# Optimization experiments

Hardware: AMD Instinct MI355X
Metric: run time of the kernel (lower is better)

## Reference

```python
import jax, jax.numpy as jnp
import numpy as np

EMBED_DIM = 1024
NUM_HEADS = 16
D_K = EMBED_DIM // NUM_HEADS
BATCH, SEQ = 4, 2048


def setup_inputs() -> dict:
    key = jax.random.key(0)
    ks = jax.random.split(key, 6)
    s = 1.0 / np.sqrt(EMBED_DIM)
    return {
        "x": jax.random.normal(ks[0], (BATCH, SEQ, EMBED_DIM), dtype=jnp.float32),
        "mask": jnp.ones((BATCH, SEQ), dtype=jnp.int32),
        "Wq": jax.random.uniform(ks[1], (EMBED_DIM, EMBED_DIM), jnp.float32, -s, s),
        "Wk": jax.random.uniform(ks[2], (EMBED_DIM, EMBED_DIM), jnp.float32, -s, s),
        "Wv": jax.random.uniform(ks[3], (EMBED_DIM, EMBED_DIM), jnp.float32, -s, s),
        "Wo": jax.random.uniform(ks[4], (EMBED_DIM, EMBED_DIM), jnp.float32, -s, s),
    }


def reference(x, mask, Wq, Wk, Wv, Wo):
    B, S, E = x.shape
    H, Dk = NUM_HEADS, D_K
    # nn.Linear: y = x @ W.T ; reshape to [B, H, S, Dk]
    def proj(W):
        return jnp.einsum('bse,fe->bsf', x, W).reshape(B, S, H, Dk).transpose(0, 2, 1, 3)
    q, k, v = proj(Wq), proj(Wk), proj(Wv)
    scores = jnp.einsum('bhqd,bhkd->bhqk', q, k) / jnp.sqrt(jnp.float32(Dk))
    # key-padding mask: [B, S] -> [B, 1, 1, S]; 0 means masked with -inf
    scores = jnp.where(mask[:, None, None, :] == 0, -jnp.inf, scores)
    attn = jax.nn.softmax(scores, axis=-1)  # dropout is identity (p=0 / eval)
    out = jnp.einsum('bhqk,bhkd->bhqd', attn, v)
    out = out.transpose(0, 2, 1, 3).reshape(B, S, E)
    return jnp.einsum('bse,fe->bsf', out, Wo)
```

## Files before the change

### kernel.cpp

```cpp
#include <hip/hip_runtime.h>

typedef __attribute__((ext_vector_type(8))) __bf16   bf16x8;
typedef __attribute__((ext_vector_type(8))) _Float16 f16x8;
typedef __attribute__((ext_vector_type(4))) float    f32x4;

#define MFMA_BF16 __builtin_amdgcn_mfma_f32_16x16x32_bf16
#define MFMA_F16  __builtin_amdgcn_mfma_f32_16x16x32_f16

__global__ __launch_bounds__(256)
void cast_bf16(const float* __restrict__ src, __bf16* __restrict__ dst, int n8)
{
    int i = blockIdx.x * 256 + threadIdx.x;
    if (i >= n8) return;
    float4 v0 = *(const float4*)(src + (size_t)i * 8);
    float4 v1 = *(const float4*)(src + (size_t)i * 8 + 4);
    float xs[8] = {v0.x, v0.y, v0.z, v0.w, v1.x, v1.y, v1.z, v1.w};
    bf16x8 h8;
    #pragma unroll
    for (int j = 0; j < 8; j++) h8[j] = (__bf16)xs[j];
    *(bf16x8*)(dst + (size_t)i * 8) = h8;
}

#define GEMM_DECLS                                                          \
    __shared__ __bf16 Ah[128][40], Bh[128][40];                             \
    const int t    = threadIdx.x;                                           \
    const int lane = t & 63;                                                \
    const int wid  = t >> 6;                                                \
    const int l15  = lane & 15;                                             \
    const int lg   = lane >> 4;                                             \
    const int wr   = wid >> 1, wc = wid & 1;

#define GEMM_LOOP(Ag, Bg, m0, brow0, K)                                     \
    f32x4 acc[4][4];                                                        \
    _Pragma("unroll")                                                       \
    for (int i = 0; i < 4; i++)                                             \
        _Pragma("unroll")                                                   \
        for (int jj = 0; jj < 4; jj++)                                      \
            _Pragma("unroll")                                               \
            for (int r = 0; r < 4; r++) acc[i][jj][r] = 0.f;                \
    for (int k0 = 0; k0 < K; k0 += 32) {                                    \
        __syncthreads();                                                    \
        _Pragma("unroll")                                                   \
        for (int i = 0; i < 2; i++) {                                       \
            int id = t + 256 * i;                                           \
            int row = id >> 2, cc = id & 3;                                 \
            *(bf16x8*)&Ah[row][cc*8] =                                      \
                *(const bf16x8*)(Ag + (size_t)(m0 + row) * K + k0 + cc*8);  \
            *(bf16x8*)&Bh[row][cc*8] =                                      \
                *(const bf16x8*)(Bg + (size_t)(brow0 + row) * K + k0 + cc*8);\
        }                                                                   \
        __syncthreads();                                                    \
        bf16x8 ah[4];                                                       \
        _Pragma("unroll")                                                   \
        for (int mr = 0; mr < 4; mr++)                                      \
            ah[mr] = *(const bf16x8*)&Ah[wr*64 + mr*16 + l15][lg*8];        \
        _Pragma("unroll")                                                   \
        for (int nr = 0; nr < 4; nr++) {                                    \
            bf16x8 bh = *(const bf16x8*)&Bh[wc*64 + nr*16 + l15][lg*8];     \
            _Pragma("unroll")                                               \
            for (int mr = 0; mr < 4; mr++)                                  \
                acc[mr][nr] = MFMA_BF16(ah[mr], bh, acc[mr][nr], 0, 0, 0);  \
        }                                                                   \
    }

__global__ __launch_bounds__(256, 4)
void gemm_qkv(const __bf16* __restrict__ xh, const __bf16* __restrict__ w3,
              __bf16* __restrict__ qh, __bf16* __restrict__ kh,
              _Float16* __restrict__ vh)
{
    GEMM_DECLS
    const int K = 1024, N = 1024;
    const int m0     = blockIdx.x * 128;
    const int by     = blockIdx.y;
    const int region = by >> 3;
    const int n0     = (by & 7) * 128;
    const int brow0  = region * 1024 + n0;
    GEMM_LOOP(xh, w3, m0, brow0, K)

    #pragma unroll
    for (int mr = 0; mr < 4; mr++)
    #pragma unroll
    for (int r = 0; r < 4; r++) {
        int row = m0 + wr*64 + mr*16 + lg*4 + r;
        #pragma unroll
        for (int nr = 0; nr < 4; nr++) {
            int col = n0 + wc*64 + nr*16 + l15;
            size_t off = (size_t)row * N + col;
            float v = acc[mr][nr][r];
            if (region == 0)      qh[off] = (__bf16)(v * 0.125f);
            else if (region == 1) kh[off] = (__bf16)v;
            else                  vh[off] = (_Float16)v;
        }
    }
}

__global__ __launch_bounds__(256, 4)
void gemm_out(const __bf16* __restrict__ aoh, const __bf16* __restrict__ woh,
              float* __restrict__ out, int M, int N, int K)
{
    GEMM_DECLS
    const int m0 = blockIdx.x * 128, n0 = blockIdx.y * 128;
    GEMM_LOOP(aoh, woh, m0, n0, K)

    #pragma unroll
    for (int mr = 0; mr < 4; mr++)
    #pragma unroll
    for (int r = 0; r < 4; r++) {
        int row = m0 + wr*64 + mr*16 + lg*4 + r;
        #pragma unroll
        for (int nr = 0; nr < 4; nr++) {
            int col = n0 + wc*64 + nr*16 + l15;
            out[(size_t)row * N + col] = acc[mr][nr][r];
        }
    }
}

__global__ __launch_bounds__(256, 2)
void attn_bf16(const __bf16* __restrict__ Qg, const __bf16* __restrict__ Kg,
               const _Float16* __restrict__ Vg, const int* __restrict__ mask,
               __bf16* AO)
{
    const int S = 2048, E = 1024;
    __shared__ __bf16   Kh[64][72];
    __shared__ _Float16 Vt[64][72];
    __shared__ _Float16 Ps[128][72];

    const int tid  = threadIdx.x;
    const int lane = tid & 63;
    const int wid  = tid >> 6;
    const int l15  = lane & 15;
    const int lg   = lane >> 4;

    const int fid = blockIdx.x;
    const int xcd = fid & 7;
    const int j   = fid >> 3;
    const int bh  = xcd * 8 + (j >> 4);
    const int qb  = j & 15;
    const int h   = bh & 15;
    const int b   = bh >> 4;
    const int q0  = qb * 128;
    const size_t base = (size_t)b * S * E + (size_t)h * 64;

    bf16x8 qf[2][2];
    #pragma unroll
    for (int mg = 0; mg < 2; mg++) {
        size_t qoff = base + (size_t)(q0 + wid*32 + mg*16 + l15) * E;
        #pragma unroll
        for (int kc = 0; kc < 2; kc++)
            qf[mg][kc] = *(const bf16x8*)(Qg + qoff + kc*32 + lg*8);
    }

    f32x4 o[2][4];
    float lpart[2][4];
    #pragma unroll
    for (int mg = 0; mg < 2; mg++)
        #pragma unroll
        for (int nt = 0; nt < 4; nt++) {
            #pragma unroll
            for (int r = 0; r < 4; r++) o[mg][nt][r] = 0.f;
            lpart[mg][nt] = 0.f;
        }

    unsigned short* Pu = (unsigned short*)&Ps[0][0];

    for (int k0 = 0; k0 < S; k0 += 64) {
        __syncthreads();

        #pragma unroll
        for (int i = 0; i < 2; i++) {
            int id  = tid + 256 * i;
            int row = id >> 3, scc = id & 7;
            size_t goff = base + (size_t)(k0 + row) * E + scc * 8;
            *(bf16x8*)&Kh[row][scc*8] = *(const bf16x8*)(Kg + goff);
            f16x8 v8 = *(const f16x8*)(Vg + goff);
            int cbase = ((row >> 3) ^ scc) * 8 + (row & 7);
            #pragma unroll
            for (int jj = 0; jj < 8; jj++)
                Vt[scc*8 + jj][cbase] = v8[jj];
        }
        __syncthreads();

        f32x4 sf[2][4];
        #pragma unroll
        for (int mg = 0; mg < 2; mg++)
            #pragma unroll
            for (int nt = 0; nt < 4; nt++)
                #pragma unroll
                for (int r = 0; r < 4; r++) sf[mg][nt][r] = 0.f;

        #pragma unroll
        for (int kc = 0; kc < 2; kc++)
            #pragma unroll
            for (int nt = 0; nt < 4; nt++) {
                bf16x8 kb = *(const bf16x8*)&Kh[nt*16 + l15][kc*32 + lg*8];
                #pragma unroll
                for (int mg = 0; mg < 2; mg++)
                    sf[mg][nt] = MFMA_BF16(qf[mg][kc], kb, sf[mg][nt], 0, 0, 0);
            }

        int mk[4];
        #pragma unroll
        for (int nt = 0; nt < 4; nt++) mk[nt] = mask[b * S + k0 + nt*16 + l15];

        #pragma unroll
        for (int mg = 0; mg < 2; mg++)
            #pragma unroll
            for (int r = 0; r < 4; r++) {
                int rowp = wid*32 + mg*16 + lg*4 + r;
                #pragma unroll
                for (int nt = 0; nt < 4; nt++) {
                    float p = mk[nt] ? __expf(sf[mg][nt][r]) : 0.f;
                    lpart[mg][r] += p;
                    _Float16 pv = (_Float16)p;
                    Pu[rowp * 72 + nt*16 + l15] = *(unsigned short*)&pv;
                }
            }

        asm volatile("s_waitcnt lgkmcnt(0)" ::: "memory");
        __builtin_amdgcn_sched_barrier(0);

        #pragma unroll
        for (int kc = 0; kc < 2; kc++) {
            f16x8 pa0 = *(const f16x8*)&Ps[wid*32 +      l15][kc*32 + lg*8];
            f16x8 pa1 = *(const f16x8*)&Ps[wid*32 + 16 + l15][kc*32 + lg*8];
            #pragma unroll
            for (int nt = 0; nt < 4; nt++) {
                int c8p = (kc*4 + lg) ^ (nt*2 + (l15 >> 3));
                f16x8 vb = *(const f16x8*)&Vt[nt*16 + l15][c8p*8];
                o[0][nt] = MFMA_F16(pa0, vb, o[0][nt], 0, 0, 0);
                o[1][nt] = MFMA_F16(pa1, vb, o[1][nt], 0, 0, 0);
            }
        }
    }

    float inv[2][4];
    #pragma unroll
    for (int mg = 0; mg < 2; mg++)
        #pragma unroll
        for (int r = 0; r < 4; r++) {
            float l = lpart[mg][r];
            #pragma unroll
            for (int d = 1; d < 16; d <<= 1) l += __shfl_xor(l, d, 16);
            inv[mg][r] = 1.0f / l;
        }

    __syncthreads();
    #pragma unroll
    for (int mg = 0; mg < 2; mg++)
        #pragma unroll
        for (int r = 0; r < 4; r++)
            #pragma unroll
            for (int nt = 0; nt < 4; nt++) {
                __bf16 v = (__bf16)(o[mg][nt][r] * inv[mg][r]);
                Pu[(wid*32 + mg*16 + lg*4 + r) * 72 + nt*16 + l15] =
                    *(unsigned short*)&v;
            }
    __syncthreads();
    #pragma unroll
    for (int i = 0; i < 4; i++) {
        int u   = tid + 256 * i;
        int row = u >> 3, c8 = u & 7;
        bf16x8 v8;
        #pragma unroll
        for (int jj = 0; jj < 8; jj++) {
            unsigned short us = Pu[row * 72 + c8*8 + jj];
            v8[jj] = *(__bf16*)&us;
        }
        *(bf16x8*)(AO + base + (size_t)(q0 + row) * E + c8 * 8) = v8;
    }
}

extern "C" void kernel_launch(void* const* d_in, const int* in_sizes, int n_in,
                              void* d_out, int out_size, void* d_ws, size_t ws_size,
                              hipStream_t stream)
{
    const float* x    = (const float*)d_in[0];
    const int*   mask = (const int*)  d_in[1];
    const float* Wq   = (const float*)d_in[2];
    const float* Wk   = (const float*)d_in[3];
    const float* Wv   = (const float*)d_in[4];
    const float* Wo   = (const float*)d_in[5];
    float* out = (float*)d_out;

    const int B = 4, S = 2048, E = 1024;
    const int M = B * S;
    const size_t SZ  = (size_t)M * E;
    const size_t WSZ = (size_t)E * E;
    const size_t PB  = SZ * sizeof(__bf16);

    char* ws = (char*)d_ws;
    __bf16*   qh = (__bf16*)(ws);
    __bf16*   kh = (__bf16*)(ws + PB);
    _Float16* vh = (_Float16*)(ws + 2*PB);
    __bf16*   xh = (__bf16*)(ws + 3*PB);
    __bf16*   w3 = (__bf16*)(ws + 4*PB);
    __bf16*   wo = (__bf16*)(ws + 4*PB + 3*WSZ*sizeof(__bf16));

    const int n8x = (int)(SZ / 8);
    const int n8w = (int)(WSZ / 8);

    cast_bf16<<<n8x/256, 256, 0, stream>>>(x,  xh, n8x);
    cast_bf16<<<n8w/256, 256, 0, stream>>>(Wq, w3,           n8w);
    cast_bf16<<<n8w/256, 256, 0, stream>>>(Wk, w3 + WSZ,     n8w);
    cast_bf16<<<n8w/256, 256, 0, stream>>>(Wv, w3 + 2*WSZ,   n8w);
    cast_bf16<<<n8w/256, 256, 0, stream>>>(Wo, wo, n8w);

    gemm_qkv<<<dim3(M/128, 24), dim3(256), 0, stream>>>(xh, w3, qh, kh, vh);

    attn_bf16<<<dim3(1024), dim3(256), 0, stream>>>(qh, kh, vh, mask, qh);

    gemm_out<<<dim3(M/128, E/128), dim3(256), 0, stream>>>(qh, wo, out, M, E, E);
}
```

Baseline: 232.7 us.

## Prefetch next K/V tile into registers and permute key order for vector P stores

Global loads for the next 64-key K/V tile are issued into registers while the current tile is processed, so memory latency overlaps with the MFMA work. K rows are permuted in shared memory so each lane's four score columns map to contiguous keys. That lets the mask load as a single int4 and the P values be written with one 4-wide store instead of four scalar 16-bit stores. The cost is more registers for the prefetch buffers, which can reduce occupancy.

```diff
diff --git a/kernel.cpp b/kernel.cpp
--- a/kernel.cpp
+++ b/kernel.cpp
@@ -2,6 +2,7 @@
 
 typedef __attribute__((ext_vector_type(8))) __bf16   bf16x8;
 typedef __attribute__((ext_vector_type(8))) _Float16 f16x8;
+typedef __attribute__((ext_vector_type(4))) _Float16 f16x4;
 typedef __attribute__((ext_vector_type(4))) float    f32x4;
 
 #define MFMA_BF16 __builtin_amdgcn_mfma_f32_16x16x32_bf16
@@ -161,22 +162,38 @@
             lpart[mg][nt] = 0.f;
         }
 
-    unsigned short* Pu = (unsigned short*)&Ps[0][0];
-
-    for (int k0 = 0; k0 < S; k0 += 64) {
+    bf16x8 kpre[2]; f16x8 vpre[2];
+    #pragma unroll
+    for (int i = 0; i < 2; i++) {
+        int id = tid + 256 * i, row = id >> 3, scc = id & 7;
+        size_t g0 = base + (size_t)(row) * E + scc * 8;
+        kpre[i] = *(const bf16x8*)(Kg + g0);
+        vpre[i] = *(const f16x8*)(Vg + g0);
+    }
+
+    const int NT = S / 64;
+    for (int t = 0; t < NT; t++) {
+        const int k0 = t * 64;
         __syncthreads();
 
         #pragma unroll
         for (int i = 0; i < 2; i++) {
-            int id  = tid + 256 * i;
-            int row = id >> 3, scc = id & 7;
-            size_t goff = base + (size_t)(k0 + row) * E + scc * 8;
-            *(bf16x8*)&Kh[row][scc*8] = *(const bf16x8*)(Kg + goff);
-            f16x8 v8 = *(const f16x8*)(Vg + goff);
+            int id = tid + 256 * i, row = id >> 3, scc = id & 7;
+            *(bf16x8*)&Kh[(row & 3) * 16 + (row >> 2)][scc*8] = kpre[i];
             int cbase = ((row >> 3) ^ scc) * 8 + (row & 7);
             #pragma unroll
             for (int jj = 0; jj < 8; jj++)
-                Vt[scc*8 + jj][cbase] = v8[jj];
+                Vt[scc*8 + jj][cbase] = vpre[i][jj];
+        }
+
+        if (t + 1 < NT) {
+            #pragma unroll
+            for (int i = 0; i < 2; i++) {
+                int id = tid + 256 * i, row = id >> 3, scc = id & 7;
+                size_t gn = base + (size_t)(k0 + 64 + row) * E + scc * 8;
+                kpre[i] = *(const bf16x8*)(Kg + gn);
+                vpre[i] = *(const f16x8*)(Vg + gn);
+            }
         }
         __syncthreads();
 
@@ -198,22 +215,22 @@
                     sf[mg][nt] = MFMA_BF16(qf[mg][kc], kb, sf[mg][nt], 0, 0, 0);
             }
 
-        int mk[4];
-        #pragma unroll
-        for (int nt = 0; nt < 4; nt++) mk[nt] = mask[b * S + k0 + nt*16 + l15];
+        int4 mk4 = *(const int4*)(mask + b * S + k0 + l15 * 4);
+        int mk[4] = {mk4.x, mk4.y, mk4.z, mk4.w};
 
         #pragma unroll
         for (int mg = 0; mg < 2; mg++)
             #pragma unroll
             for (int r = 0; r < 4; r++) {
                 int rowp = wid*32 + mg*16 + lg*4 + r;
+                f16x4 pv4;
                 #pragma unroll
                 for (int nt = 0; nt < 4; nt++) {
                     float p = mk[nt] ? __expf(sf[mg][nt][r]) : 0.f;
                     lpart[mg][r] += p;
-                    _Float16 pv = (_Float16)p;
-                    Pu[rowp * 72 + nt*16 + l15] = *(unsigned short*)&pv;
+                    pv4[nt] = (_Float16)p;
                 }
+                *(f16x4*)&Ps[rowp][l15 * 4] = pv4;
             }
 
         asm volatile("s_waitcnt lgkmcnt(0)" ::: "memory");
@@ -244,6 +261,7 @@
             inv[mg][r] = 1.0f / l;
         }
 
+    unsigned short* Pu = (unsigned short*)&Ps[0][0];
     __syncthreads();
     #pragma unroll
     for (int mg = 0; mg < 2; mg++)
```

Measured after the change: 218.5 us. -6.1%, faster.
